# Kernel tuning notes

Measured on AMD Instinct MI355X. Metric: run time of the kernel, lower is better.

Reference implementation:

```python
import jax, jax.numpy as jnp
import numpy as np

B = 4096   # batch
F = 100    # input_size (number of per-feature NAM backbones)
H = 128    # hidden_size
H2 = H // 2
T = 2      # num_treatment


def setup_inputs() -> dict:
    key = jax.random.key(0)
    ks = jax.random.split(key, 16)
    s = 1.0 / np.sqrt(H)
    inp = {
        "x": jax.random.normal(ks[0], (B, F), dtype=jnp.float32),
        "a": jax.random.randint(ks[1], (B,), 0, T),
        "W1": jax.random.normal(ks[2], (F, H), dtype=jnp.float32),
        "b1": jax.random.normal(ks[3], (F, H), dtype=jnp.float32) * 0.01,
        "W2": jax.random.normal(ks[4], (F, H, H), dtype=jnp.float32) * s,
        "b2": jax.random.normal(ks[5], (F, H), dtype=jnp.float32) * 0.01,
        "W3": jax.random.normal(ks[6], (F, H, H), dtype=jnp.float32) * s,
        "b3": jax.random.normal(ks[7], (F, H), dtype=jnp.float32) * 0.01,
        "W4": jax.random.normal(ks[8], (F, H, H), dtype=jnp.float32) * s,
        "b4": jax.random.normal(ks[9], (F, H), dtype=jnp.float32) * 0.01,
        # heads: per treatment, Linear(H, H/2) -> Linear(H/2, 1), stacked over [F, T]
        "Wh1": jax.random.normal(ks[10], (F, T, H, H2), dtype=jnp.float32) * s,
        "bh1": jax.random.normal(ks[11], (F, T, H2), dtype=jnp.float32) * 0.01,
        "Wh2": jax.random.normal(ks[12], (F, T, H2), dtype=jnp.float32) * (1.0 / np.sqrt(H2)),
        "bh2": jax.random.normal(ks[13], (F, T), dtype=jnp.float32) * 0.01,
    }
    return inp


def reference(x, a, W1, b1, W2, b2, W3, b3, W4, b4, Wh1, bh1, Wh2, bh2):
    # Per-feature tiny MLP backbones, batched over the feature axis F.
    h = jax.nn.elu(x[:, :, None] * W1[None] + b1[None])           # [B,F,H]
    h = jax.nn.elu(jnp.einsum('bfh,fhk->bfk', h, W2) + b2[None])  # [B,F,H]
    h = jax.nn.elu(jnp.einsum('bfh,fhk->bfk', h, W3) + b3[None])  # [B,F,H]
    bb = jnp.einsum('bfh,fhk->bfk', h, W4) + b4[None]             # [B,F,H], no ELU on last layer
    backbone_sum = bb.sum(axis=1)                                  # [B,H]
    # Two-linear heads per treatment (no nonlinearity between, as in source)
    hid = jnp.einsum('bfh,fthm->bftm', bb, Wh1) + bh1[None]       # [B,F,T,H2]
    y = jnp.einsum('bftm,ftm->bft', hid, Wh2) + bh2[None]         # [B,F,T]
    # Gather treatment-indexed prediction per sample, sum over features
    y_sel = jnp.take_along_axis(y, a[:, None, None].astype(jnp.int32), axis=2)[..., 0]  # [B,F]
    sum_out = y_sel.sum(axis=1, keepdims=True)                     # [B,1]
    return (backbone_sum, sum_out)
```

## Files before the change

kernel.cpp:

```cpp
#include <hip/hip_runtime.h>
#include <hip/hip_bf16.h>
#include <math.h>

#define B_  4096
#define F_  100
#define H_  128
#define H2_ 64
#define NG  16

typedef float    f32x4  __attribute__((ext_vector_type(4)));
typedef __bf16   bf16x8 __attribute__((ext_vector_type(8)));
typedef __bf16   bf16x2 __attribute__((ext_vector_type(2)));
typedef unsigned int uint4v __attribute__((ext_vector_type(4)));

__device__ __forceinline__ float el(float v) { return v > 0.f ? v : __expf(v) - 1.f; }

__device__ __forceinline__ unsigned pkpair(float lo, float hi) {
  bf16x2 t; t[0] = (__bf16)lo; t[1] = (__bf16)hi;
  return __builtin_bit_cast(unsigned, t);
}

__global__ __launch_bounds__(256) void prep(
    const float* __restrict__ W2, const float* __restrict__ W3, const float* __restrict__ W4,
    const float* __restrict__ Wh1, const float* __restrict__ bh1,
    const float* __restrict__ Wh2, const float* __restrict__ bh2,
    const float* __restrict__ x,
    __bf16* __restrict__ wb, float* __restrict__ wv, float* __restrict__ cb,
    float* __restrict__ xT) {
  const int bid = blockIdx.x;
  const int tid = threadIdx.x;
  if (bid < 300) {
    __shared__ __align__(16) float tile[128 * 132];
    const int f = bid / 3, ly = bid % 3;
    const float* src = (ly == 0 ? W2 : (ly == 1 ? W3 : W4)) + (size_t)f * (H_ * H_);
    #pragma unroll
    for (int r = 0; r < 16; ++r) {
      int i4 = tid + 256 * r;
      int k = i4 >> 5, n0 = (i4 & 31) << 2;
      *(f32x4*)&tile[k * 132 + n0] = *(const f32x4*)(src + ((size_t)i4 << 2));
    }
    __syncthreads();
    bf16x8 o[8]; int bo[8];
    #pragma unroll
    for (int wq = 0; wq < 8; ++wq) {
      int idx = tid + 256 * wq;
      int n = idx >> 4, c = idx & 15;
      #pragma unroll
      for (int j = 0; j < 8; ++j) o[wq][j] = (__bf16)tile[(8 * c + j) * 132 + n];
      bo[wq] = ((n << 8) + (c << 4)) ^ ((n & 7) << 4);
    }
    __syncthreads();
    char* obuf = (char*)tile;
    #pragma unroll
    for (int wq = 0; wq < 8; ++wq) *(bf16x8*)(obuf + bo[wq]) = o[wq];
    __syncthreads();
    char* wo = (char*)(wb + (size_t)bid * (H_ * H_));
    #pragma unroll
    for (int w = 0; w < 8; ++w) {
      int off = (tid + 256 * w) * 16;
      *(bf16x8*)(wo + off) = *(const bf16x8*)(obuf + off);
    }
  } else if (bid < 500) {
    const int hb = bid - 300;
    __shared__ __align__(16) float w2s[H2_];
    if (tid < 64) w2s[tid] = Wh2[hb * H2_ + tid];
    __syncthreads();
    const int h = tid >> 1, half = tid & 1;
    const f32x4* rw = (const f32x4*)(Wh1 + ((size_t)hb * H_ + h) * H2_ + half * 32);
    const f32x4* bvp = (const f32x4*)&w2s[half * 32];
    float s = 0.f;
    #pragma unroll
    for (int m4 = 0; m4 < 8; ++m4) {
      f32x4 av = rw[m4], bv = bvp[m4];
      s += av[0]*bv[0] + av[1]*bv[1] + av[2]*bv[2] + av[3]*bv[3];
    }
    s += __shfl_xor(s, 1);
    if (!half) wv[hb * H_ + h] = s;
    if (tid < 64) {
      float p = bh1[hb * H2_ + tid] * w2s[tid];
      #pragma unroll
      for (int off = 32; off > 0; off >>= 1) p += __shfl_xor(p, off);
      if (tid == 0) cb[hb] = p + bh2[hb];
    }
  } else {
    const int r = (bid - 500) * 256 + tid;
    const f32x4* src = (const f32x4*)(x + (size_t)r * F_);
    #pragma unroll 5
    for (int j4 = 0; j4 < F_ / 4; ++j4) {
      f32x4 v = src[j4];
      #pragma unroll
      for (int c = 0; c < 4; ++c) xT[(size_t)(j4 * 4 + c) * B_ + r] = v[c];
    }
  }
}

__device__ __forceinline__ bf16x8 lda(const __bf16* buf, int mt, int ks, int lc, int g) {
  int rown = mt * 16 + lc;
  int boff = (rown << 8) + (ks << 6) + (g << 4);
  boff ^= (rown & 7) << 4;
  return *(const bf16x8*)((const char*)buf + boff);
}

__device__ __forceinline__ bf16x8 exch(const unsigned (&pks)[8][2], int ks, int s0l, bool hi5) {
  unsigned a0 = __shfl(pks[2*ks][0],   s0l,      64);
  unsigned a1 = __shfl(pks[2*ks][1],   s0l,      64);
  unsigned b0 = __shfl(pks[2*ks+1][0], s0l,      64);
  unsigned b1 = __shfl(pks[2*ks+1][1], s0l,      64);
  unsigned c0 = __shfl(pks[2*ks][0],   s0l + 16, 64);
  unsigned c1 = __shfl(pks[2*ks][1],   s0l + 16, 64);
  unsigned d0 = __shfl(pks[2*ks+1][0], s0l + 16, 64);
  unsigned d1 = __shfl(pks[2*ks+1][1], s0l + 16, 64);
  uint4v u;
  u[0] = hi5 ? b0 : a0;  u[1] = hi5 ? b1 : a1;
  u[2] = hi5 ? d0 : c0;  u[3] = hi5 ? d1 : c1;
  return __builtin_bit_cast(bf16x8, u);
}

#define PHASE_SYNC() do {                                                   \
    asm volatile("s_waitcnt lgkmcnt(0)" ::: "memory");                      \
    __builtin_amdgcn_s_barrier();                                           \
    if (item + 2 < nitems) {                                                \
      stage(item + 2);                                                      \
      asm volatile("s_waitcnt vmcnt(8)" ::: "memory");                      \
    } else {                                                                \
      asm volatile("s_waitcnt vmcnt(0)" ::: "memory");                      \
    }                                                                       \
    __builtin_amdgcn_s_barrier();                                           \
    ++item;                                                                 \
  } while (0)

__global__ __launch_bounds__(256, 2) void nam_mfma(
    const float* __restrict__ xT, const int* __restrict__ a,
    const float* __restrict__ W1, const float* __restrict__ b1,
    const float* __restrict__ b2, const float* __restrict__ b3, const float* __restrict__ b4,
    const float* __restrict__ wv, const float* __restrict__ cb,
    const __bf16* __restrict__ wb,
    float* __restrict__ pbb, float* __restrict__ py) {
  __shared__ __align__(1024) __bf16 wlds[2][H_ * H_];

  const int tid = threadIdx.x;
  const int l  = tid & 63;
  const int lc = l & 15, g = l >> 4;
  const int by = blockIdx.x;
  const int rw = blockIdx.y * 128 + (tid >> 6) * 32;
  const int f0 = (by * F_) / NG, f1 = ((by + 1) * F_) / NG;
  const int nitems = 3 * (f1 - f0);

  const int row0 = rw + lc, row1 = rw + 16 + lc;
  const int ta0 = a[row0], ta1 = a[row1];
  const int s0l = lc + ((l & 16) << 1);
  const bool hi5 = (l & 32) != 0;

  f32x4 acc[8][2], bbsum[8][2];
  unsigned pk[2][8][2];
  const f32x4 z = {0.f, 0.f, 0.f, 0.f};
  #pragma unroll
  for (int mt = 0; mt < 8; ++mt) { bbsum[mt][0] = z; bbsum[mt][1] = z; }
  float ysum0 = 0.f, ysum1 = 0.f;

  auto stage = [&](int it) {
    const char* gsrc = (const char*)(wb + (size_t)(f0 * 3 + it) * (H_ * H_));
    char* ldst = (char*)&wlds[it & 1][0];
    #pragma unroll
    for (int r = 0; r < 8; ++r) {
      int off = (tid + 256 * r) * 16;
      __builtin_amdgcn_global_load_lds(
          (const __attribute__((address_space(1))) void*)(gsrc + off),
          (__attribute__((address_space(3))) void*)(ldst + off), 16, 0, 0);
    }
  };

  stage(0); stage(1);
  asm volatile("s_waitcnt vmcnt(8)" ::: "memory");
  __builtin_amdgcn_s_barrier();

  int item = 0;
  for (int fi = f0; fi < f1; ++fi) {
    {
      const __bf16* buf = wlds[item & 1];
      #pragma unroll
      for (int mt = 0; mt < 8; ++mt) { acc[mt][0] = z; acc[mt][1] = z; }
      const float* w1p = W1 + (size_t)fi * H_;
      const float* b1p = b1 + (size_t)fi * H_;
      float xs0 = xT[(size_t)fi * B_ + row0];
      float xs1 = xT[(size_t)fi * B_ + row1];
      #pragma unroll
      for (int ks = 0; ks < 4; ++ks) {
        int k0 = ks * 32 + 8 * g;
        f32x4 wa  = *(const f32x4*)(w1p + k0);
        f32x4 wb2 = *(const f32x4*)(w1p + k0 + 4);
        f32x4 ba  = *(const f32x4*)(b1p + k0);
        f32x4 bb2 = *(const f32x4*)(b1p + k0 + 4);
        bf16x8 bf0, bf1;
        #pragma unroll
        for (int e = 0; e < 4; ++e) {
          bf0[e]     = (__bf16)el(xs0 * wa[e]  + ba[e]);
          bf0[e + 4] = (__bf16)el(xs0 * wb2[e] + bb2[e]);
          bf1[e]     = (__bf16)el(xs1 * wa[e]  + ba[e]);
          bf1[e + 4] = (__bf16)el(xs1 * wb2[e] + bb2[e]);
        }
        #pragma unroll
        for (int mt = 0; mt < 8; ++mt) {
          bf16x8 av = lda(buf, mt, ks, lc, g);
          acc[mt][0] = __builtin_amdgcn_mfma_f32_16x16x32_bf16(av, bf0, acc[mt][0], 0, 0, 0);
          acc[mt][1] = __builtin_amdgcn_mfma_f32_16x16x32_bf16(av, bf1, acc[mt][1], 0, 0, 0);
        }
      }
      const float* bp = b2 + (size_t)fi * H_;
      #pragma unroll
      for (int mt = 0; mt < 8; ++mt) {
        f32x4 bia = *(const f32x4*)(bp + mt * 16 + 4 * g);
        #pragma unroll
        for (int nt = 0; nt < 2; ++nt) {
          f32x4 t = acc[mt][nt];
          float t0 = el(t[0] + bia[0]), t1 = el(t[1] + bia[1]);
          float t2 = el(t[2] + bia[2]), t3 = el(t[3] + bia[3]);
          pk[nt][mt][0] = pkpair(t0, t1);
          pk[nt][mt][1] = pkpair(t2, t3);
        }
      }
    }
    PHASE_SYNC();
    {
      const __bf16* buf = wlds[item & 1];
      #pragma unroll
      for (int mt = 0; mt < 8; ++mt) { acc[mt][0] = z; acc[mt][1] = z; }
      #pragma unroll
      for (int ks = 0; ks < 4; ++ks) {
        bf16x8 bf0 = exch(pk[0], ks, s0l, hi5);
        bf16x8 bf1 = exch(pk[1], ks, s0l, hi5);
        #pragma unroll
        for (int mt = 0; mt < 8; ++mt) {
          bf16x8 av = lda(buf, mt, ks, lc, g);
          acc[mt][0] = __builtin_amdgcn_mfma_f32_16x16x32_bf16(av, bf0, acc[mt][0], 0, 0, 0);
          acc[mt][1] = __builtin_amdgcn_mfma_f32_16x16x32_bf16(av, bf1, acc[mt][1], 0, 0, 0);
        }
      }
      const float* bp = b3 + (size_t)fi * H_;
      #pragma unroll
      for (int mt = 0; mt < 8; ++mt) {
        f32x4 bia = *(const f32x4*)(bp + mt * 16 + 4 * g);
        #pragma unroll
        for (int nt = 0; nt < 2; ++nt) {
          f32x4 t = acc[mt][nt];
          float t0 = el(t[0] + bia[0]), t1 = el(t[1] + bia[1]);
          float t2 = el(t[2] + bia[2]), t3 = el(t[3] + bia[3]);
          pk[nt][mt][0] = pkpair(t0, t1);
          pk[nt][mt][1] = pkpair(t2, t3);
        }
      }
    }
    PHASE_SYNC();
    {
      const __bf16* buf = wlds[item & 1];
      #pragma unroll
      for (int mt = 0; mt < 8; ++mt) { acc[mt][0] = z; acc[mt][1] = z; }
      #pragma unroll
      for (int ks = 0; ks < 4; ++ks) {
        bf16x8 bf0 = exch(pk[0], ks, s0l, hi5);
        bf16x8 bf1 = exch(pk[1], ks, s0l, hi5);
        #pragma unroll
        for (int mt = 0; mt < 8; ++mt) {
          bf16x8 av = lda(buf, mt, ks, lc, g);
          acc[mt][0] = __builtin_amdgcn_mfma_f32_16x16x32_bf16(av, bf0, acc[mt][0], 0, 0, 0);
          acc[mt][1] = __builtin_amdgcn_mfma_f32_16x16x32_bf16(av, bf1, acc[mt][1], 0, 0, 0);
        }
      }
      const float* b4p = b4 + (size_t)fi * H_;
      const float* wv0 = wv + (size_t)(fi * 2 + ta0) * H_;
      const float* wv1 = wv + (size_t)(fi * 2 + ta1) * H_;
      float yd0 = 0.f, yd1 = 0.f;
      #pragma unroll
      for (int mt = 0; mt < 8; ++mt) {
        int n = mt * 16 + 4 * g;
        f32x4 bia = *(const f32x4*)(b4p + n);
        f32x4 v0 = acc[mt][0] + bia;
        f32x4 v1 = acc[mt][1] + bia;
        bbsum[mt][0] += v0;
        bbsum[mt][1] += v1;
        f32x4 wa = *(const f32x4*)(wv0 + n);
        f32x4 wc = *(const f32x4*)(wv1 + n);
        yd0 += v0[0]*wa[0] + v0[1]*wa[1] + v0[2]*wa[2] + v0[3]*wa[3];
        yd1 += v1[0]*wc[0] + v1[1]*wc[1] + v1[2]*wc[2] + v1[3]*wc[3];
      }
      ysum0 += yd0 + (g == 0 ? cb[fi * 2 + ta0] : 0.f);
      ysum1 += yd1 + (g == 0 ? cb[fi * 2 + ta1] : 0.f);
    }
    PHASE_SYNC();
  }

  #pragma unroll
  for (int mt = 0; mt < 8; ++mt) {
    int n = mt * 16 + 4 * g;
    *(f32x4*)(pbb + ((size_t)by * B_ + row0) * H_ + n) = bbsum[mt][0];
    *(f32x4*)(pbb + ((size_t)by * B_ + row1) * H_ + n) = bbsum[mt][1];
  }
  float y0 = ysum0 + __shfl_xor(ysum0, 16, 64); y0 += __shfl_xor(y0, 32, 64);
  float y1 = ysum1 + __shfl_xor(ysum1, 16, 64); y1 += __shfl_xor(y1, 32, 64);
  if (g == 0) {
    py[by * B_ + row0] = y0;
    py[by * B_ + row1] = y1;
  }
}

__global__ __launch_bounds__(256) void reduce_out(const float* __restrict__ pbb,
                                                  const float* __restrict__ py,
                                                  float* __restrict__ out) {
  const int base = (blockIdx.x * 256 + threadIdx.x) * 4;
  f32x4 s = {0.f, 0.f, 0.f, 0.f};
  if (base < B_ * H_) {
    #pragma unroll
    for (int g = 0; g < NG; ++g) s += *(const f32x4*)(pbb + (size_t)g * (B_ * H_) + base);
  } else {
    const int b = base - B_ * H_;
    #pragma unroll
    for (int g = 0; g < NG; ++g) s += *(const f32x4*)(py + g * B_ + b);
  }
  *(f32x4*)(out + base) = s;
}

extern "C" void kernel_launch(void* const* d_in, const int* in_sizes, int n_in,
                              void* d_out, int out_size, void* d_ws, size_t ws_size,
                              hipStream_t stream) {
  const float* x   = (const float*)d_in[0];
  const int*   aa  = (const int*)d_in[1];
  const float* W1  = (const float*)d_in[2];
  const float* b1  = (const float*)d_in[3];
  const float* W2  = (const float*)d_in[4];
  const float* b2  = (const float*)d_in[5];
  const float* W3  = (const float*)d_in[6];
  const float* b3  = (const float*)d_in[7];
  const float* W4  = (const float*)d_in[8];
  const float* b4  = (const float*)d_in[9];
  const float* Wh1 = (const float*)d_in[10];
  const float* bh1 = (const float*)d_in[11];
  const float* Wh2 = (const float*)d_in[12];
  const float* bh2 = (const float*)d_in[13];
  float* out = (float*)d_out;

  char* ws = (char*)d_ws;
  float*  wv  = (float*)(ws + 0);
  float*  cbp = (float*)(ws + 102400);
  __bf16* wbp = (__bf16*)(ws + 103424);
  float*  xT  = (float*)(ws + 9933824);
  float*  py  = (float*)(ws + 11572224);
  float*  pbb = (float*)(ws + 11834368);

  prep<<<dim3(516), dim3(256), 0, stream>>>(W2, W3, W4, Wh1, bh1, Wh2, bh2, x,
                                            wbp, wv, cbp, xT);
  nam_mfma<<<dim3(NG, B_ / 128), dim3(256), 0, stream>>>(
      xT, aa, W1, b1, b2, b3, b4, wv, cbp, wbp, pbb, py);
  reduce_out<<<dim3((B_ * H_ + B_) / 1024), dim3(256), 0, stream>>>(pbb, py, out);
}
```

Measured before the change: 227.4 us.

## Fuse final reduction into main kernel and drop x transpose pass

Removes the separate reduce_out kernel. The last block to finish for each batch tile, detected with a per-tile atomic counter that prep zeroes, sums the per-feature-group partials and writes the output directly. The transpose of x in prep is also removed, so the main kernel reads x with a stride instead. The grid dimensions are swapped, so blocks for the same feature group are scheduled next to each other. The aim is to save one kernel launch plus a pass over the transposed data, at the cost of strided x loads and a serialized tail reduction. There is no threadfence before the atomic, so visibility of other blocks' partials is not formally guaranteed.

```diff
diff --git a/kernel.cpp b/kernel.cpp
--- a/kernel.cpp
+++ b/kernel.cpp
@@ -24,11 +24,11 @@
     const float* __restrict__ W2, const float* __restrict__ W3, const float* __restrict__ W4,
     const float* __restrict__ Wh1, const float* __restrict__ bh1,
     const float* __restrict__ Wh2, const float* __restrict__ bh2,
-    const float* __restrict__ x,
     __bf16* __restrict__ wb, float* __restrict__ wv, float* __restrict__ cb,
-    float* __restrict__ xT) {
+    unsigned* __restrict__ rctr) {
   const int bid = blockIdx.x;
   const int tid = threadIdx.x;
+  if (bid == 0 && tid < 32) rctr[tid] = 0u;
   if (bid < 300) {
     __shared__ __align__(16) float tile[128 * 132];
     const int f = bid / 3, ly = bid % 3;
@@ -60,7 +60,7 @@
       int off = (tid + 256 * w) * 16;
       *(bf16x8*)(wo + off) = *(const bf16x8*)(obuf + off);
     }
-  } else if (bid < 500) {
+  } else {
     const int hb = bid - 300;
     __shared__ __align__(16) float w2s[H2_];
     if (tid < 64) w2s[tid] = Wh2[hb * H2_ + tid];
@@ -81,15 +81,6 @@
       #pragma unroll
       for (int off = 32; off > 0; off >>= 1) p += __shfl_xor(p, off);
       if (tid == 0) cb[hb] = p + bh2[hb];
-    }
-  } else {
-    const int r = (bid - 500) * 256 + tid;
-    const f32x4* src = (const f32x4*)(x + (size_t)r * F_);
-    #pragma unroll 5
-    for (int j4 = 0; j4 < F_ / 4; ++j4) {
-      f32x4 v = src[j4];
-      #pragma unroll
-      for (int c = 0; c < 4; ++c) xT[(size_t)(j4 * 4 + c) * B_ + r] = v[c];
     }
   }
 }
@@ -130,19 +121,22 @@
   } while (0)
 
 __global__ __launch_bounds__(256, 2) void nam_mfma(
-    const float* __restrict__ xT, const int* __restrict__ a,
+    const float* __restrict__ x, const int* __restrict__ a,
     const float* __restrict__ W1, const float* __restrict__ b1,
     const float* __restrict__ b2, const float* __restrict__ b3, const float* __restrict__ b4,
     const float* __restrict__ wv, const float* __restrict__ cb,
     const __bf16* __restrict__ wb,
-    float* __restrict__ pbb, float* __restrict__ py) {
+    float* __restrict__ pbb, float* __restrict__ py,
+    unsigned* __restrict__ rctr, float* __restrict__ out) {
   __shared__ __align__(1024) __bf16 wlds[2][H_ * H_];
+  __shared__ int winner_flag;
 
   const int tid = threadIdx.x;
   const int l  = tid & 63;
   const int lc = l & 15, g = l >> 4;
-  const int by = blockIdx.x;
-  const int rw = blockIdx.y * 128 + (tid >> 6) * 32;
+  const int bx = blockIdx.x;
+  const int by = blockIdx.y;
+  const int rw = bx * 128 + (tid >> 6) * 32;
   const int f0 = (by * F_) / NG, f1 = ((by + 1) * F_) / NG;
   const int nitems = 3 * (f1 - f0);
 
@@ -182,8 +176,8 @@
       for (int mt = 0; mt < 8; ++mt) { acc[mt][0] = z; acc[mt][1] = z; }
       const float* w1p = W1 + (size_t)fi * H_;
       const float* b1p = b1 + (size_t)fi * H_;
-      float xs0 = xT[(size_t)fi * B_ + row0];
-      float xs1 = xT[(size_t)fi * B_ + row1];
+      float xs0 = x[(size_t)row0 * F_ + fi];
+      float xs1 = x[(size_t)row1 * F_ + fi];
       #pragma unroll
       for (int ks = 0; ks < 4; ++ks) {
         int k0 = ks * 32 + 8 * g;
@@ -301,22 +295,32 @@
     py[by * B_ + row0] = y0;
     py[by * B_ + row1] = y1;
   }
-}
-
-__global__ __launch_bounds__(256) void reduce_out(const float* __restrict__ pbb,
-                                                  const float* __restrict__ py,
-                                                  float* __restrict__ out) {
-  const int base = (blockIdx.x * 256 + threadIdx.x) * 4;
-  f32x4 s = {0.f, 0.f, 0.f, 0.f};
-  if (base < B_ * H_) {
-    #pragma unroll
-    for (int g = 0; g < NG; ++g) s += *(const f32x4*)(pbb + (size_t)g * (B_ * H_) + base);
-  } else {
-    const int b = base - B_ * H_;
-    #pragma unroll
-    for (int g = 0; g < NG; ++g) s += *(const f32x4*)(py + g * B_ + b);
-  }
-  *(f32x4*)(out + base) = s;
+
+  __syncthreads();
+  if (tid == 0) {
+    unsigned old = atomicAdd(&rctr[bx], 1u);
+    winner_flag = (old == NG - 1) ? 1 : 0;
+  }
+  __syncthreads();
+  if (winner_flag) {
+    const int fbase = bx * 128 * H_;
+    #pragma unroll
+    for (int k = 0; k < 16; ++k) {
+      int v4 = tid + 256 * k;
+      int base = fbase + v4 * 4;
+      f32x4 s = z;
+      #pragma unroll
+      for (int gg = 0; gg < NG; ++gg) s += *(const f32x4*)(pbb + (size_t)gg * (B_ * H_) + base);
+      *(f32x4*)(out + base) = s;
+    }
+    if (tid < 32) {
+      int base = bx * 128 + tid * 4;
+      f32x4 s = z;
+      #pragma unroll
+      for (int gg = 0; gg < NG; ++gg) s += *(const f32x4*)(py + gg * B_ + base);
+      *(f32x4*)(out + B_ * H_ + base) = s;
+    }
+  }
 }
 
 extern "C" void kernel_launch(void* const* d_in, const int* in_sizes, int n_in,
@@ -339,16 +343,15 @@
   float* out = (float*)d_out;
 
   char* ws = (char*)d_ws;
-  float*  wv  = (float*)(ws + 0);
-  float*  cbp = (float*)(ws + 102400);
-  __bf16* wbp = (__bf16*)(ws + 103424);
-  float*  xT  = (float*)(ws + 9933824);
-  float*  py  = (float*)(ws + 11572224);
-  float*  pbb = (float*)(ws + 11834368);
-
-  prep<<<dim3(516), dim3(256), 0, stream>>>(W2, W3, W4, Wh1, bh1, Wh2, bh2, x,
-                                            wbp, wv, cbp, xT);
-  nam_mfma<<<dim3(NG, B_ / 128), dim3(256), 0, stream>>>(
-      xT, aa, W1, b1, b2, b3, b4, wv, cbp, wbp, pbb, py);
-  reduce_out<<<dim3((B_ * H_ + B_) / 1024), dim3(256), 0, stream>>>(pbb, py, out);
-}
+  float*    wv   = (float*)(ws + 0);
+  float*    cbp  = (float*)(ws + 102400);
+  unsigned* rctr = (unsigned*)(ws + 103296);
+  __bf16*   wbp  = (__bf16*)(ws + 103424);
+  float*    py   = (float*)(ws + 9933824);
+  float*    pbb  = (float*)(ws + 10195968);
+
+  prep<<<dim3(500), dim3(256), 0, stream>>>(W2, W3, W4, Wh1, bh1, Wh2, bh2,
+                                            wbp, wv, cbp, rctr);
+  nam_mfma<<<dim3(32, NG), dim3(256), 0, stream>>>(
+      x, aa, W1, b1, b2, b3, b4, wv, cbp, wbp, pbb, py, rctr, out);
+}
```

Measured after the change: 238.9 us. 5.1% more time.
